# Kernel optimization log

Measured on AMD Instinct MI355X. Metric: run time of the kernel, lower is better.

The kernel has to match this reference:

```python
import jax, jax.numpy as jnp
import numpy as np

D_MODEL = 2048
D_HID = 4096
N_EXPERTS = 8
TOP_K = 2
B, S = 2, 2048


def setup_inputs() -> dict:
    key = jax.random.key(0)
    ks = jax.random.split(key, 4)
    x = jax.random.normal(ks[0], (B, S, D_MODEL), dtype=jnp.float32)
    router_w = jax.random.normal(ks[1], (D_MODEL, N_EXPERTS), dtype=jnp.float32) * (D_MODEL ** -0.5)
    w1 = jax.random.normal(ks[2], (N_EXPERTS, D_MODEL, D_HID), dtype=jnp.float32) * (D_MODEL ** -0.5)
    b1 = jnp.zeros((N_EXPERTS, D_HID), dtype=jnp.float32)
    w2 = jax.random.normal(ks[3], (N_EXPERTS, D_HID, D_MODEL), dtype=jnp.float32) * (D_HID ** -0.5)
    b2 = jnp.zeros((N_EXPERTS, D_MODEL), dtype=jnp.float32)
    return {"x": x, "router_w": router_w, "w1": w1, "b1": b1, "w2": w2, "b2": b2}


def reference(x, router_w, w1, b1, w2, b2):
    # x: [B, S, D] -> tokens [T, D]
    Bc, Sc, D = x.shape
    xt = x.reshape(-1, D)                      # [T, D]
    T = xt.shape[0]
    E = w1.shape[0]

    # --- TopKRouter: linear gate -> softmax -> top-k, renormalized weights ---
    logits = xt @ router_w                     # [T, E]
    probs = jax.nn.softmax(logits, axis=-1)    # [T, E]
    weights, indices = jax.lax.top_k(probs, TOP_K)  # [T, K]
    weights = weights / jnp.sum(weights, axis=-1, keepdims=True)

    # Combine weights per (token, expert): sum over k-slots of weight * 1[idx==e]
    combine = jnp.zeros((T, E), dtype=xt.dtype).at[
        jnp.arange(T)[:, None], indices
    ].add(weights)                             # [T, E]

    # --- Expert FFNs: Linear -> GELU (exact, torch default) -> Linear ---
    out = jnp.zeros_like(xt)
    for e in range(E):  # small fixed loop over experts
        h = jax.nn.gelu(xt @ w1[e] + b1[e], approximate=False)  # [T, H]
        y = h @ w2[e] + b2[e]                                   # [T, D]
        out = out + combine[:, e:e + 1] * y

    return out.reshape(Bc, Sc, D)
```

## Files before the change

### kernel.cpp

```cpp
#include <hip/hip_runtime.h>

typedef unsigned short u16;
typedef unsigned int u32;
typedef short bf16x8 __attribute__((ext_vector_type(8)));
typedef float f32x4 __attribute__((ext_vector_type(4)));

#define T_TOK 4096
#define DM 2048
#define DH 4096
#define NE 8
#define MAXSLOT 9216
#define MAXTILE 72

#define OFF_META   128
#define OFF_TILEE  192
#define OFF_TOPE   512
#define OFF_TOPW   33280
#define OFF_SLOTT  66048
#define OFF_UNION  102912
#define OFF_XBF    139776
#define OFF_W1T    16916992ULL
#define OFF_W2T    151134720ULL
#define OFF_Y      285352448ULL
#define OFF_H3     323101184ULL
#define NEED_Y     324149760ULL

__device__ __forceinline__ u16 f2bf(float f) {
  union { float f; u32 u; } v; v.f = f;
  u32 r = v.u + 0x7fffu + ((v.u >> 16) & 1u);
  return (u16)(r >> 16);
}

__device__ __forceinline__ float bf2f(u16 h) {
  union { u32 u; float f; } v; v.u = ((u32)h) << 16; return v.f;
}

__device__ __forceinline__ float f4c(const float4& v, int c) {
  return c == 0 ? v.x : c == 1 ? v.y : c == 2 ? v.z : v.w;
}

__device__ __forceinline__ void gl_lds16(const u16* g, u16* l) {
  typedef __attribute__((address_space(1))) const u32 gu32;
  typedef __attribute__((address_space(3))) u32 lu32;
  __builtin_amdgcn_global_load_lds((gu32*)(const void*)g, (lu32*)(void*)l, 16, 0, 0);
}

__device__ __forceinline__ float gelu_f(float v) {
  float x = v * 0.70710678118654752f;
  float ax = fabsf(x);
  float t = 1.0f / fmaf(0.3275911f, ax, 1.0f);
  float p = t * fmaf(t, fmaf(t, fmaf(t, fmaf(t, 1.061405429f, -1.453152027f),
                                     1.421413741f), -0.284496736f), 0.254829592f);
  float er = 1.0f - p * __expf(-x * x);
  er = copysignf(er, x);
  return 0.5f * v * (1.0f + er);
}

__global__ __launch_bounds__(256) void prep_kernel(
    const float* __restrict__ x, const float* __restrict__ rw,
    const float* __restrict__ w1, const float* __restrict__ w2,
    int* __restrict__ counts, int* __restrict__ top_e, float* __restrict__ top_w,
    u16* __restrict__ xbf, u16* __restrict__ w1t, u16* __restrict__ w2t)
{
  __shared__ u16 T_s[4][64][64];
  int bid = blockIdx.x;
  if (bid < 8192) {
    const float* W; u16* Wt; int K, N, k0, n0;
    if (bid < 4096) {
      int e = bid >> 9, r = bid & 511;
      W = w1 + (size_t)e * DM * DH; Wt = w1t + (size_t)e * DM * DH;
      K = DM; N = DH; k0 = (r >> 4) * 64; n0 = (r & 15) * 256;
    } else {
      int b2 = bid - 4096;
      int e = b2 >> 9, r = b2 & 511;
      W = w2 + (size_t)e * DM * DH; Wt = w2t + (size_t)e * DM * DH;
      K = DH; N = DM; k0 = (r >> 3) * 64; n0 = (r & 7) * 256;
    }
    int wv = threadIdx.x >> 6, l = threadIdx.x & 63;
    int nw = n0 + wv * 64;
    const float* src = W + (size_t)k0 * N + nw + l;
#pragma unroll
    for (int h = 0; h < 2; ++h) {
      float v[32];
#pragma unroll
      for (int i = 0; i < 32; ++i) v[i] = src[(size_t)(h * 32 + i) * N];
#pragma unroll
      for (int j = 0; j < 4; ++j) {
        uint4 pk;
        pk.x = f2bf(v[j * 8 + 0]) | ((u32)f2bf(v[j * 8 + 1]) << 16);
        pk.y = f2bf(v[j * 8 + 2]) | ((u32)f2bf(v[j * 8 + 3]) << 16);
        pk.z = f2bf(v[j * 8 + 4]) | ((u32)f2bf(v[j * 8 + 5]) << 16);
        pk.w = f2bf(v[j * 8 + 6]) | ((u32)f2bf(v[j * 8 + 7]) << 16);
        int slot = ((h * 4 + j) + l) & 7;
        *(uint4*)&T_s[wv][l][slot * 8] = pk;
      }
    }
    __syncthreads();
#pragma unroll
    for (int r2 = 0; r2 < 8; ++r2) {
      int row = r2 * 8 + (l >> 3);
      int slot = ((l & 7) + row) & 7;
      uint4 vv = *(const uint4*)&T_s[wv][row][slot * 8];
      *(uint4*)(Wt + (size_t)(nw + row) * K + k0 + (l & 7) * 8) = vv;
    }
  } else {
    int wv = threadIdx.x >> 6;
    int lane = threadIdx.x & 63;
    int t = (bid - 8192) * 4 + wv;
    const float4* xr = (const float4*)(x + (size_t)t * DM);
    const float4* rw4 = (const float4*)rw;
    float acc[NE];
#pragma unroll
    for (int e = 0; e < NE; ++e) acc[e] = 0.f;
    for (int i = 0; i < 8; ++i) {
      int d4 = i * 64 + lane;
      float4 xv = xr[d4];
      uint2 pk;
      pk.x = f2bf(xv.x) | ((u32)f2bf(xv.y) << 16);
      pk.y = f2bf(xv.z) | ((u32)f2bf(xv.w) << 16);
      *(uint2*)(xbf + (size_t)t * DM + d4 * 4) = pk;
#pragma unroll
      for (int j = 0; j < 4; ++j) {
        int d = 4 * d4 + j;
        float4 r0 = rw4[d * 2];
        float4 r1 = rw4[d * 2 + 1];
        float xs = f4c(xv, j);
        acc[0] += xs * r0.x; acc[1] += xs * r0.y; acc[2] += xs * r0.z; acc[3] += xs * r0.w;
        acc[4] += xs * r1.x; acc[5] += xs * r1.y; acc[6] += xs * r1.z; acc[7] += xs * r1.w;
      }
    }
#pragma unroll
    for (int off = 32; off > 0; off >>= 1)
#pragma unroll
      for (int e = 0; e < NE; ++e) acc[e] += __shfl_xor(acc[e], off, 64);
    if (lane == 0) {
      int e0 = 0; float l0 = acc[0];
#pragma unroll
      for (int e = 1; e < NE; ++e) if (acc[e] > l0) { l0 = acc[e]; e0 = e; }
      int e1 = -1; float l1 = -3.0e38f;
#pragma unroll
      for (int e = 0; e < NE; ++e) if (e != e0 && acc[e] > l1) { l1 = acc[e]; e1 = e; }
      float w0 = 1.f / (1.f + expf(l1 - l0));
      float w1v = 1.f - w0;
      top_e[t * 2 + 0] = e0; top_e[t * 2 + 1] = e1;
      top_w[t * 2 + 0] = w0; top_w[t * 2 + 1] = w1v;
      atomicAdd(&counts[e0], 1);
      atomicAdd(&counts[e1], 1);
    }
  }
}

__global__ void scan_kernel(int* __restrict__ wsI)
{
  int* counts = wsI;
  int* curs   = wsI + 8;
  int* offs   = wsI + 16;
  int* meta   = wsI + (OFF_META / 4);
  int* tile_e = wsI + (OFF_TILEE / 4);
  int* slot_token = wsI + (OFF_SLOTT / 4);
  float* slot_wt = (float*)(wsI + (OFF_UNION / 4));
  __shared__ int s_off[9];
  if (threadIdx.x == 0) {
    int o = 0;
    for (int e = 0; e < NE; ++e) {
      offs[e] = o; curs[e] = o; s_off[e] = o;
      o += (counts[e] + 127) & ~127;
    }
    offs[8] = o; s_off[8] = o;
    meta[0] = o >> 7;
  }
  __syncthreads();
  int nt = s_off[8] >> 7;
  for (int i = threadIdx.x; i < MAXTILE; i += blockDim.x) {
    int e = -1;
    if (i < nt) {
      for (int j = 0; j < NE; ++j)
        if (i * 128 >= s_off[j] && i * 128 < s_off[j + 1]) e = j;
    }
    tile_e[i] = e;
  }
  for (int i = threadIdx.x; i < MAXSLOT; i += blockDim.x) {
    slot_token[i] = -1;
    slot_wt[i] = 0.f;
  }
}

__global__ void scatter_kernel(const int* __restrict__ top_e, const float* __restrict__ top_w,
                               int* __restrict__ curs, int* __restrict__ slot_token,
                               int* __restrict__ tok_slots, float* __restrict__ slot_wt,
                               int useY)
{
  int t = blockIdx.x * blockDim.x + threadIdx.x;
  if (t >= T_TOK) return;
#pragma unroll
  for (int k = 0; k < 2; ++k) {
    int e = top_e[t * 2 + k];
    int pos = atomicAdd(&curs[e], 1);
    slot_token[pos] = t;
    if (useY) tok_slots[t * 2 + k] = pos;
    else      slot_wt[pos] = top_w[t * 2 + k];
  }
}


#define GATEN(n) asm volatile("s_waitcnt vmcnt(" #n ")" ::: "memory")
#define NOGATE ((void)0)
#define NOSTG  ((void)0)
#define NORD   ((void)0)

#define SA_(PA, KO) do { \
  gl_lds16(aptr0 + (KO), &PA[wid * 16][0]);        \
  gl_lds16(aptr1 + (KO), &PA[64 + wid * 16][0]); } while (0)
#define SB1_(PB, KO) gl_lds16(bptr0 + (KO), &PB[wid * 16][0])
#define SB2_(PB, KO) do { \
  gl_lds16(bptr1 + (KO), &PB[64 + wid * 16][0]);   \
  gl_lds16(bptr2 + (KO), &PB[128 + wid * 16][0]);  \
  gl_lds16(bptr3 + (KO), &PB[192 + wid * 16][0]); } while (0)

#define RDAF8(P)                                                        \
  _Pragma("unroll")                                                     \
  for (int i_ = 0; i_ < 8; ++i_)                                        \
    af[i_] = *(const bf16x8*)&P[i_ * 16 + lrow][sp8]
#define RDBF(P)                                                         \
  _Pragma("unroll")                                                     \
  for (int n_ = 0; n_ < 4; ++n_)                                        \
    bfr[n_] = *(const bf16x8*)&P[wn + n_ * 16 + lrow][sp8]

#define PHF(STG, GATE, RD) do {                                         \
  STG;                                                                  \
  GATE;                                                                 \
  __builtin_amdgcn_s_barrier();                                         \
  asm volatile("s_waitcnt lgkmcnt(0)" ::: "memory");                    \
  __builtin_amdgcn_sched_barrier(0);                                    \
  __builtin_amdgcn_s_setprio(1);                                        \
  _Pragma("unroll")                                                     \
  for (int nf = 0; nf < 4; ++nf)                                        \
    _Pragma("unroll")                                                   \
    for (int mf = 0; mf < 8; ++mf)                                      \
      acc[nf][mf] = __builtin_amdgcn_mfma_f32_16x16x32_bf16(            \
          bfr[nf], af[mf], acc[nf][mf], 0, 0, 0);                       \
  __builtin_amdgcn_s_setprio(0);                                        \
  RD;                                                                   \
  __builtin_amdgcn_s_barrier();                                         \
  __builtin_amdgcn_sched_barrier(0);                                    \
} while (0)

template<int MODE, int EPI>
__global__ __launch_bounds__(256, 2) void gemm_tb(
    const u16* __restrict__ Wt, const float* __restrict__ bias,
    const u16* __restrict__ Abase,
    u16* __restrict__ Hout, u16* __restrict__ Ybuf, float* __restrict__ Out,
    const int* __restrict__ slot_token, const float* __restrict__ slot_wt,
    const int* __restrict__ tile_e, const int* __restrict__ meta,
    int tile0, int mtc)
{
  constexpr int KD = (MODE == 0) ? DM : DH;
  constexpr int ND = (MODE == 0) ? DH : DM;
  constexpr int NT = ND / 256;
  constexpr int NK = KD / 32;

  __shared__ u16 A_s[3][128][32];
  __shared__ u16 B_s[3][256][32];

  int nwg = gridDim.x;
  int flat = blockIdx.x;
  int q8 = nwg >> 3, rr = nwg & 7;
  int xcd = flat & 7, i0 = flat >> 3;
  int wg = (xcd < rr ? xcd * (q8 + 1) : rr * (q8 + 1) + (xcd - rr) * q8) + i0;
  int mloc = wg / NT;
  int ntile = wg % NT;
  int mt = tile0 + mloc;
  if (mt >= meta[0]) return;
  int e = tile_e[mt];
  int n0 = ntile * 256;

  const int tid = threadIdx.x;
  const int lane = tid & 63;
  const int wid = tid >> 6;
  const int lrow = lane & 15;
  const int g = lane >> 4;
  const int sp8 = (g ^ ((lrow >> 1) & 3)) << 3;
  const int wn = wid << 6;

  const int srow = tid >> 2;
  const int swz = ((tid & 3) ^ ((tid >> 3) & 3)) << 3;

  const u16 *aptr0, *aptr1;
  if (MODE == 0) {
    int t0 = slot_token[mt * 128 + srow];       if (t0 < 0) t0 = 0;
    int t1 = slot_token[mt * 128 + 64 + srow];  if (t1 < 0) t1 = 0;
    aptr0 = Abase + (size_t)t0 * KD + swz;
    aptr1 = Abase + (size_t)t1 * KD + swz;
  } else {
    aptr0 = Abase + (size_t)(mloc * 128 + srow) * KD + swz;
    aptr1 = Abase + (size_t)(mloc * 128 + 64 + srow) * KD + swz;
  }
  const u16* bptr0 = Wt + ((size_t)e * ND + n0 + srow) * KD + swz;
  const u16* bptr1 = bptr0 + (size_t)64 * KD;
  const u16* bptr2 = bptr0 + (size_t)128 * KD;
  const u16* bptr3 = bptr0 + (size_t)192 * KD;

  f32x4 acc[4][8] = {};
  bf16x8 af[8], bfr[4];

  u16 (*pA0)[32] = A_s[0]; u16 (*pA1)[32] = A_s[1]; u16 (*pA2)[32] = A_s[2];
  u16 (*pB0)[32] = B_s[0]; u16 (*pB1)[32] = B_s[1]; u16 (*pB2)[32] = B_s[2];

  SA_(pA0, 0); SB1_(pB0, 0); SB2_(pB0, 0);
  SA_(pA1, 32); SB1_(pB1, 32); SB2_(pB1, 32);
  GATEN(6);
  __builtin_amdgcn_s_barrier();
  __builtin_amdgcn_sched_barrier(0);
  RDAF8(pA0);
  RDBF(pB0);

  for (int t = 0; t < NK - 2; ++t) {
    int ko = (t + 2) * 32;
    PHF(SA_(pA2, ko); SB1_(pB2, ko); SB2_(pB2, ko), GATEN(6),
        RDAF8(pA1); RDBF(pB1));
    u16 (*tA)[32] = pA0; pA0 = pA1; pA1 = pA2; pA2 = tA;
    u16 (*tB)[32] = pB0; pB0 = pB1; pB1 = pB2; pB2 = tB;
  }
  PHF(NOSTG, GATEN(0), RDAF8(pA1); RDBF(pB1));
  PHF(NOSTG, NOGATE, NORD);

  const int rb = g << 2;
  float4 bias4[4];
#pragma unroll
  for (int nf = 0; nf < 4; ++nf)
    bias4[nf] = *(const float4*)&bias[e * ND + n0 + wn + nf * 16 + rb];

  if constexpr (MODE == 0) {
#pragma unroll
    for (int mf = 0; mf < 8; ++mf) {
      u16* hp = Hout + (size_t)(mloc * 128 + mf * 16 + lrow) * DH + n0 + wn + rb;
#pragma unroll
      for (int nf = 0; nf < 4; ++nf) {
        float v0 = gelu_f(acc[nf][mf][0] + bias4[nf].x);
        float v1 = gelu_f(acc[nf][mf][1] + bias4[nf].y);
        float v2 = gelu_f(acc[nf][mf][2] + bias4[nf].z);
        float v3 = gelu_f(acc[nf][mf][3] + bias4[nf].w);
        uint2 pk;
        pk.x = f2bf(v0) | ((u32)f2bf(v1) << 16);
        pk.y = f2bf(v2) | ((u32)f2bf(v3) << 16);
        *(uint2*)(hp + nf * 16) = pk;
      }
    }
  } else if constexpr (EPI == 0) {
#pragma unroll
    for (int mf = 0; mf < 8; ++mf) {
      u16* yp = Ybuf + (size_t)(mt * 128 + mf * 16 + lrow) * DM + n0 + wn + rb;
#pragma unroll
      for (int nf = 0; nf < 4; ++nf) {
        float v0 = acc[nf][mf][0] + bias4[nf].x;
        float v1 = acc[nf][mf][1] + bias4[nf].y;
        float v2 = acc[nf][mf][2] + bias4[nf].z;
        float v3 = acc[nf][mf][3] + bias4[nf].w;
        uint2 pk;
        pk.x = f2bf(v0) | ((u32)f2bf(v1) << 16);
        pk.y = f2bf(v2) | ((u32)f2bf(v3) << 16);
        *(uint2*)(yp + nf * 16) = pk;
      }
    }
  } else {
#pragma unroll
    for (int mf = 0; mf < 8; ++mf) {
      int gs = mt * 128 + mf * 16 + lrow;
      int tok = slot_token[gs];
      if (tok < 0) continue;
      float wt = slot_wt[gs];
      float* op = Out + (size_t)tok * DM + n0 + wn + rb;
#pragma unroll
      for (int nf = 0; nf < 4; ++nf) {
        atomicAdd(op + nf * 16 + 0, wt * (acc[nf][mf][0] + bias4[nf].x));
        atomicAdd(op + nf * 16 + 1, wt * (acc[nf][mf][1] + bias4[nf].y));
        atomicAdd(op + nf * 16 + 2, wt * (acc[nf][mf][2] + bias4[nf].z));
        atomicAdd(op + nf * 16 + 3, wt * (acc[nf][mf][3] + bias4[nf].w));
      }
    }
  }
}

__global__ __launch_bounds__(256) void combine_kernel(
    const u16* __restrict__ y, const int* __restrict__ tok_slots,
    const float* __restrict__ top_w, float* __restrict__ out)
{
  int t = blockIdx.x;
  int d = threadIdx.x * 8;
  int s0 = tok_slots[t * 2], s1 = tok_slots[t * 2 + 1];
  float w0 = top_w[t * 2], w1 = top_w[t * 2 + 1];
  union { uint4 u; u16 s[8]; } a, b;
  a.u = *(const uint4*)(y + (size_t)s0 * DM + d);
  b.u = *(const uint4*)(y + (size_t)s1 * DM + d);
  float o[8];
#pragma unroll
  for (int j = 0; j < 8; ++j) o[j] = w0 * bf2f(a.s[j]) + w1 * bf2f(b.s[j]);
  float* op = out + (size_t)t * DM + d;
  *(float4*)op = make_float4(o[0], o[1], o[2], o[3]);
  *(float4*)(op + 4) = make_float4(o[4], o[5], o[6], o[7]);
}

extern "C" void kernel_launch(void* const* d_in, const int* in_sizes, int n_in,
                              void* d_out, int out_size, void* d_ws, size_t ws_size,
                              hipStream_t stream) {
  const float* x  = (const float*)d_in[0];
  const float* rw = (const float*)d_in[1];
  const float* w1 = (const float*)d_in[2];
  const float* b1 = (const float*)d_in[3];
  const float* w2 = (const float*)d_in[4];
  const float* b2 = (const float*)d_in[5];
  float* out = (float*)d_out;
  char* ws = (char*)d_ws;

  int* counts = (int*)ws;
  int* curs   = (int*)(ws + 32);
  int* meta   = (int*)(ws + OFF_META);
  int* tile_e = (int*)(ws + OFF_TILEE);
  int* top_e  = (int*)(ws + OFF_TOPE);
  float* top_w = (float*)(ws + OFF_TOPW);
  int* slot_token = (int*)(ws + OFF_SLOTT);
  int* tok_slots  = (int*)(ws + OFF_UNION);
  float* slot_wt  = (float*)(ws + OFF_UNION);
  u16* xbf = (u16*)(ws + OFF_XBF);
  u16* w1t = (u16*)(ws + OFF_W1T);
  u16* w2t = (u16*)(ws + OFF_W2T);

  const int useY = (ws_size >= NEED_Y) ? 1 : 0;
  u16* ybuf = (u16*)(ws + OFF_Y);
  u16* hbuf = (u16*)(ws + (useY ? OFF_H3 : OFF_Y));

  hipMemsetAsync(ws, 0, 512, stream);
  if (!useY) hipMemsetAsync(d_out, 0, (size_t)out_size * sizeof(float), stream);

  prep_kernel<<<9216, 256, 0, stream>>>(x, rw, w1, w2, counts, top_e, top_w,
                                        xbf, w1t, w2t);
  scan_kernel<<<1, 256, 0, stream>>>((int*)ws);
  scatter_kernel<<<T_TOK / 256, 256, 0, stream>>>(top_e, top_w, curs, slot_token,
                                                  tok_slots, slot_wt, useY);

  size_t hoff = useY ? OFF_H3 : OFF_Y;
  size_t avail = ws_size > hoff ? ws_size - hoff : (size_t)DH * 256;
  long ch_slots = (long)(avail / (DH * 2));
  ch_slots = (ch_slots / 128) * 128;
  if (ch_slots > MAXSLOT) ch_slots = MAXSLOT;
  if (ch_slots < 128) ch_slots = 128;
  int mtc = (int)(ch_slots / 128);
  int nchunks = (MAXTILE + mtc - 1) / mtc;

  for (int c = 0; c < nchunks; ++c) {
    int tile0 = c * mtc;
    gemm_tb<0, 0><<<dim3(mtc * (DH / 256)), 256, 0, stream>>>(
        w1t, b1, xbf, hbuf, nullptr, nullptr, slot_token, slot_wt, tile_e, meta, tile0, mtc);
    if (useY) {
      gemm_tb<1, 0><<<dim3(mtc * (DM / 256)), 256, 0, stream>>>(
          w2t, b2, hbuf, nullptr, ybuf, nullptr, slot_token, slot_wt, tile_e, meta, tile0, mtc);
    } else {
      gemm_tb<1, 1><<<dim3(mtc * (DM / 256)), 256, 0, stream>>>(
          w2t, b2, hbuf, nullptr, nullptr, out, slot_token, slot_wt, tile_e, meta, tile0, mtc);
    }
  }
  if (useY)
    combine_kernel<<<T_TOK, 256, 0, stream>>>(ybuf, tok_slots, top_w, out);
}
```

Before: 700.6 us.

## Pre-tile transposed bf16 weights into contiguous per-k-step blocks for GEMM B loads

The weight prep kernel now writes the transposed bf16 weights in a tiled layout where each 256-column by 32-k block is one contiguous 8192-element chunk, already pre-swizzled to match the LDS layout. The GEMM B-operand loads then read fully contiguous memory per k-step from a single base pointer, instead of four strided row streams. This is meant to improve global load coalescing and cut address arithmetic, at the cost of a more complex prep write pattern and coupling the layout to fixed tile sizes.

```diff
diff --git a/kernel.cpp b/kernel.cpp
--- a/kernel.cpp
+++ b/kernel.cpp
@@ -65,16 +65,18 @@
   __shared__ u16 T_s[4][64][64];
   int bid = blockIdx.x;
   if (bid < 8192) {
-    const float* W; u16* Wt; int K, N, k0, n0;
+    const float* W; u16* WtT; int N, k0, n0;
     if (bid < 4096) {
       int e = bid >> 9, r = bid & 511;
-      W = w1 + (size_t)e * DM * DH; Wt = w1t + (size_t)e * DM * DH;
-      K = DM; N = DH; k0 = (r >> 4) * 64; n0 = (r & 15) * 256;
+      W = w1 + (size_t)e * DM * DH;
+      N = DH; k0 = (r >> 4) * 64; n0 = (r & 15) * 256;
+      WtT = w1t + ((size_t)((e * 16 + (r & 15)) * 64 + (r >> 4) * 2)) * 8192;
     } else {
       int b2 = bid - 4096;
       int e = b2 >> 9, r = b2 & 511;
-      W = w2 + (size_t)e * DM * DH; Wt = w2t + (size_t)e * DM * DH;
-      K = DH; N = DM; k0 = (r >> 3) * 64; n0 = (r & 7) * 256;
+      W = w2 + (size_t)e * DM * DH;
+      N = DM; k0 = (r >> 3) * 64; n0 = (r & 7) * 256;
+      WtT = w2t + ((size_t)((e * 8 + (r & 7)) * 128 + (r >> 3) * 2)) * 8192;
     }
     int wv = threadIdx.x >> 6, l = threadIdx.x & 63;
     int nw = n0 + wv * 64;
@@ -96,12 +98,19 @@
       }
     }
     __syncthreads();
-#pragma unroll
-    for (int r2 = 0; r2 < 8; ++r2) {
-      int row = r2 * 8 + (l >> 3);
-      int slot = ((l & 7) + row) & 7;
-      uint4 vv = *(const uint4*)&T_s[wv][row][slot * 8];
-      *(uint4*)(Wt + (size_t)(nw + row) * K + k0 + (l & 7) * 8) = vv;
+    int tid = threadIdx.x;
+    int lr = tid >> 2;
+    int s  = tid & 3;
+    int kf = s ^ ((tid >> 3) & 3);
+#pragma unroll
+    for (int ks_l = 0; ks_l < 2; ++ks_l) {
+      int J = ks_l * 4 + kf;
+#pragma unroll
+      for (int q = 0; q < 4; ++q) {
+        int slot = (J + lr) & 7;
+        uint4 vv = *(const uint4*)&T_s[q][lr][slot * 8];
+        *(uint4*)(WtT + (size_t)ks_l * 8192 + q * 2048 + tid * 8) = vv;
+      }
     }
   } else {
     int wv = threadIdx.x >> 6;
@@ -211,11 +220,11 @@
 #define SA_(PA, KO) do { \
   gl_lds16(aptr0 + (KO), &PA[wid * 16][0]);        \
   gl_lds16(aptr1 + (KO), &PA[64 + wid * 16][0]); } while (0)
-#define SB1_(PB, KO) gl_lds16(bptr0 + (KO), &PB[wid * 16][0])
-#define SB2_(PB, KO) do { \
-  gl_lds16(bptr1 + (KO), &PB[64 + wid * 16][0]);   \
-  gl_lds16(bptr2 + (KO), &PB[128 + wid * 16][0]);  \
-  gl_lds16(bptr3 + (KO), &PB[192 + wid * 16][0]); } while (0)
+#define SBALL(PB, KS) do { \
+  gl_lds16(bptrT + (size_t)(KS) * 8192,        &PB[wid * 16][0]);        \
+  gl_lds16(bptrT + (size_t)(KS) * 8192 + 2048, &PB[64 + wid * 16][0]);   \
+  gl_lds16(bptrT + (size_t)(KS) * 8192 + 4096, &PB[128 + wid * 16][0]);  \
+  gl_lds16(bptrT + (size_t)(KS) * 8192 + 6144, &PB[192 + wid * 16][0]); } while (0)
 
 #define RDAF8(P)                                                        \
   _Pragma("unroll")                                                     \
@@ -295,10 +304,7 @@
     aptr0 = Abase + (size_t)(mloc * 128 + srow) * KD + swz;
     aptr1 = Abase + (size_t)(mloc * 128 + 64 + srow) * KD + swz;
   }
-  const u16* bptr0 = Wt + ((size_t)e * ND + n0 + srow) * KD + swz;
-  const u16* bptr1 = bptr0 + (size_t)64 * KD;
-  const u16* bptr2 = bptr0 + (size_t)128 * KD;
-  const u16* bptr3 = bptr0 + (size_t)192 * KD;
+  const u16* bptrT = Wt + ((size_t)(e * NT + ntile) * NK) * 8192 + tid * 8;
 
   f32x4 acc[4][8] = {};
   bf16x8 af[8], bfr[4];
@@ -306,8 +312,8 @@
   u16 (*pA0)[32] = A_s[0]; u16 (*pA1)[32] = A_s[1]; u16 (*pA2)[32] = A_s[2];
   u16 (*pB0)[32] = B_s[0]; u16 (*pB1)[32] = B_s[1]; u16 (*pB2)[32] = B_s[2];
 
-  SA_(pA0, 0); SB1_(pB0, 0); SB2_(pB0, 0);
-  SA_(pA1, 32); SB1_(pB1, 32); SB2_(pB1, 32);
+  SA_(pA0, 0); SBALL(pB0, 0);
+  SA_(pA1, 32); SBALL(pB1, 1);
   GATEN(6);
   __builtin_amdgcn_s_barrier();
   __builtin_amdgcn_sched_barrier(0);
@@ -316,7 +322,7 @@
 
   for (int t = 0; t < NK - 2; ++t) {
     int ko = (t + 2) * 32;
-    PHF(SA_(pA2, ko); SB1_(pB2, ko); SB2_(pB2, ko), GATEN(6),
+    PHF(SA_(pA2, ko); SBALL(pB2, t + 2), GATEN(6),
         RDAF8(pA1); RDBF(pB1));
     u16 (*tA)[32] = pA0; pA0 = pA1; pA1 = pA2; pA2 = tA;
     u16 (*tB)[32] = pB0; pB0 = pB1; pB1 = pB2; pB2 = tB;
```

After: 671.4 us. -4.2%, faster.
